# Kernel tuning notes

Hardware: AMD Instinct MI355X
Metric: run time of the kernel (lower is better)

## Reference

```python
import jax, jax.numpy as jnp
import numpy as np

TAU = 0.1

def setup_inputs() -> dict:
    key = jax.random.key(0)
    k1, k2 = jax.random.split(key)
    z_i = jax.random.normal(k1, (4096, 1024), dtype=jnp.float32)
    z_j = jax.random.normal(k2, (4096, 1024), dtype=jnp.float32)
    return {"z_i": z_i, "z_j": z_j}

def reference(z_i, z_j):
    N = z_i.shape[0]
    # L2-normalize each view (world_size=1 so gather is identity)
    k_i = z_i / jnp.linalg.norm(z_i, axis=-1, keepdims=True)
    k_j = z_j / jnp.linalg.norm(z_j, axis=-1, keepdims=True)
    k = jnp.concatenate([k_i, k_j], axis=0)          # [2N, D]
    # cosine similarity of normalized vectors == plain dot products
    sim = k @ k.T                                     # [2N, 2N]
    # positives: (i, i+N) and (i+N, i) pairs
    sim_ij = jnp.diagonal(sim, offset=N)
    sim_ji = jnp.diagonal(sim, offset=-N)
    positives = jnp.concatenate([sim_ij, sim_ji], axis=0)  # [2N]
    # denominator masks out self-similarity on the diagonal
    mask = ~jnp.eye(2 * N, dtype=bool)
    denom = jnp.sum(jnp.where(mask, jnp.exp(sim / TAU), 0.0), axis=1)  # [2N]
    all_losses = -(positives / TAU - jnp.log(denom))
    loss = jnp.sum(all_losses) / (2 * N)
    return loss
```

## Files before the change

### kernel.cpp

```cpp
#include <hip/hip_runtime.h>
#include <hip/hip_bf16.h>
#include <cstdint>
#include <math.h>

#define D_DIM 1024
#define TAU_INV 10.0f
#define EXP_SCALE (TAU_INV / 4096.0f)
#define BK 64
#define NT (D_DIM / BK)
#define BM 256
#define BN 128
#define SLOT 24576

typedef float f32x4 __attribute__((ext_vector_type(4)));
typedef long  l64x2 __attribute__((ext_vector_type(2)));

#define VMCNT(n) asm volatile("s_waitcnt vmcnt(" #n ")" ::: "memory")
#define LGKM0()  asm volatile("s_waitcnt lgkmcnt(0)" ::: "memory")
#define BAR() do { asm volatile("" ::: "memory"); \
                   __builtin_amdgcn_s_barrier();  \
                   asm volatile("" ::: "memory"); } while (0)

__device__ __forceinline__ float wave_reduce_add(float v) {
#pragma unroll
    for (int off = 32; off > 0; off >>= 1) v += __shfl_xor(v, off, 64);
    return v;
}

__global__ __launch_bounds__(256)
void norm_pos_kernel(const float* __restrict__ zi, const float* __restrict__ zj,
                     unsigned int* __restrict__ Kf, float* __restrict__ rowsum,
                     float* __restrict__ pos, int n_half) {
    const int i = blockIdx.x;
    const int t = threadIdx.x;
    float4 a = reinterpret_cast<const float4*>(zi + (size_t)i * D_DIM)[t];
    float4 b = reinterpret_cast<const float4*>(zj + (size_t)i * D_DIM)[t];
    float ssa = a.x*a.x + a.y*a.y + a.z*a.z + a.w*a.w;
    float ssb = b.x*b.x + b.y*b.y + b.z*b.z + b.w*b.w;
    float dab = a.x*b.x + a.y*b.y + a.z*b.z + a.w*b.w;
    ssa = wave_reduce_add(ssa);
    ssb = wave_reduce_add(ssb);
    dab = wave_reduce_add(dab);
    __shared__ float wsa[4], wsb[4], wsd[4];
    if ((t & 63) == 0) { wsa[t>>6] = ssa; wsb[t>>6] = ssb; wsd[t>>6] = dab; }
    __syncthreads();
    const float inva = 1.0f / sqrtf(wsa[0] + wsa[1] + wsa[2] + wsa[3]);
    const float invb = 1.0f / sqrtf(wsb[0] + wsb[1] + wsb[2] + wsb[3]);
    const float sa = inva * 64.0f;
    const float sb = invb * 64.0f;
    unsigned int ua = 0, ub = 0;
    ua = __builtin_amdgcn_cvt_pk_fp8_f32(a.x * sa, a.y * sa, ua, false);
    ua = __builtin_amdgcn_cvt_pk_fp8_f32(a.z * sa, a.w * sa, ua, true);
    ub = __builtin_amdgcn_cvt_pk_fp8_f32(b.x * sb, b.y * sb, ub, false);
    ub = __builtin_amdgcn_cvt_pk_fp8_f32(b.z * sb, b.w * sb, ub, true);
    const int w = (t >> 4) * 16 + ((t >> 1) & 3) * 4 + ((t >> 3) & 1) * 2 + (t & 1);
    Kf[(size_t)i * 256 + w] = ua;
    Kf[(size_t)(i + n_half) * 256 + w] = ub;
    if (t == 0) {
        pos[i] = (wsd[0] + wsd[1] + wsd[2] + wsd[3]) * inva * invb;
        rowsum[i] = 0.0f;
        rowsum[i + n_half] = 0.0f;
    }
}

__global__ __launch_bounds__(512, 4)
void simclr_gemm_kernel(const unsigned char* __restrict__ Kmat,
                        float* __restrict__ rowsum, int n_total) {
    __shared__ char lds[73728];

    const int tid  = threadIdx.x;
    const int lane = tid & 63;
    const int wave = tid >> 6;
    const int wr = wave >> 1;
    const int wc = wave & 1;
    const int kgrp = lane >> 4;

    const int wg = (blockIdx.x & 7) * 132 + (blockIdx.x >> 3);

    int by = 0, start = 0;
    while (wg >= start + (64 - 2 * by)) { start += 64 - 2 * by; ++by; }
    const int bx = 2 * by + (wg - start);
    const bool diag = ((bx >> 1) == by);
    const int rowbase = by * BM;
    const int colbase = bx * BN;

    const char* gK = reinterpret_cast<const char*>(Kmat);
    const int srow = tid >> 2;
    const int sswz = (tid & 3) ^ ((srow >> 1) & 3);

    auto stage_all = [&](int tt) {
        const int s = tt % 3;
        const size_t kbyte = (size_t)tt * BK;
        char* dstA = lds + s * SLOT + tid * 16;
        char* dstB = lds + s * SLOT + 16384 + tid * 16;
#pragma unroll
        for (int i = 0; i < 2; ++i) {
            const int row = i * 128 + srow;
            const char* src = gK + (size_t)(rowbase + row) * D_DIM + kbyte + sswz * 16;
            __builtin_amdgcn_global_load_lds(
                (const __attribute__((address_space(1))) void*)src,
                (__attribute__((address_space(3))) void*)(dstA + i * 8192),
                16, 0, 0);
        }
        {
            const char* src = gK + (size_t)(colbase + srow) * D_DIM + kbyte + sswz * 16;
            __builtin_amdgcn_global_load_lds(
                (const __attribute__((address_space(1))) void*)src,
                (__attribute__((address_space(3))) void*)dstB,
                16, 0, 0);
        }
    };

    f32x4 acc[4][4] = {};
    l64x2 af[4], bf[4];

    auto read_frag = [&](const char* base, int row) -> l64x2 {
        return *reinterpret_cast<const l64x2*>(
            base + row * 64 + ((kgrp ^ ((row >> 1) & 3)) << 4));
    };

    stage_all(0); stage_all(1);
    VMCNT(3); BAR();

    for (int t = 0; t < NT; ++t) {
        const int s = t % 3;
        const char* Ab = lds + s * SLOT;
        const char* Bb = Ab + 16384;
#pragma unroll
        for (int mi = 0; mi < 4; ++mi)
            af[mi] = read_frag(Ab, wr * 64 + mi * 16 + (lane & 15));
#pragma unroll
        for (int ni = 0; ni < 4; ++ni)
            bf[ni] = read_frag(Bb, wc * 64 + ni * 16 + (lane & 15));
        if (t + 2 < NT) stage_all(t + 2);
        __builtin_amdgcn_s_setprio(1);
#pragma unroll
        for (int mi = 0; mi < 4; ++mi)
#pragma unroll
            for (int ni = 0; ni < 4; ++ni)
                acc[mi][ni] = __builtin_amdgcn_mfma_f32_16x16x32_fp8_fp8(
                    af[mi].x, bf[ni].x, acc[mi][ni], 0, 0, 0);
        __builtin_amdgcn_s_setprio(0);
        if (t < NT - 1) {
            LGKM0();
            if (t < NT - 2) { VMCNT(3); } else { VMCNT(0); }
            BAR();
        }
        __builtin_amdgcn_s_setprio(1);
#pragma unroll
        for (int mi = 0; mi < 4; ++mi)
#pragma unroll
            for (int ni = 0; ni < 4; ++ni)
                acc[mi][ni] = __builtin_amdgcn_mfma_f32_16x16x32_fp8_fp8(
                    af[mi].y, bf[ni].y, acc[mi][ni], 0, 0, 0);
        __builtin_amdgcn_s_setprio(0);
    }

    float colpart[4] = {0.0f, 0.0f, 0.0f, 0.0f};
#pragma unroll
    for (int mi = 0; mi < 4; ++mi) {
#pragma unroll
        for (int reg = 0; reg < 4; ++reg) {
            const int grow = rowbase + wr * 64 + mi * 16 + ((lane >> 4) << 2) + reg;
            float rowpart = 0.0f;
#pragma unroll
            for (int ni = 0; ni < 4; ++ni) {
                const int gcol = colbase + wc * 64 + ni * 16 + (lane & 15);
                float e = __expf(acc[mi][ni][reg] * EXP_SCALE);
                if (diag && grow == gcol) e = 0.0f;
                rowpart += e;
                colpart[ni] += e;
            }
#pragma unroll
            for (int off = 1; off < 16; off <<= 1)
                rowpart += __shfl_xor(rowpart, off, 64);
            if ((lane & 15) == 0) atomicAdd(&rowsum[grow], rowpart);
        }
    }
    if (!diag) {
#pragma unroll
        for (int ni = 0; ni < 4; ++ni) {
            float cp = colpart[ni];
            cp += __shfl_xor(cp, 16, 64);
            cp += __shfl_xor(cp, 32, 64);
            if (lane < 16)
                atomicAdd(&rowsum[colbase + wc * 64 + ni * 16 + lane], cp);
        }
    }
}

__global__ __launch_bounds__(256)
void loss_kernel(const float* __restrict__ rowsum, const float* __restrict__ pos,
                 float* __restrict__ out, int n_total, int n_half) {
    const int t = threadIdx.x;
    float acc = 0.0f;
    for (int r = t; r < n_total; r += 256) {
        const int pi = (r < n_half) ? r : (r - n_half);
        acc += logf(rowsum[r]) - TAU_INV * pos[pi];
    }
    acc = wave_reduce_add(acc);
    __shared__ float ws4[4];
    if ((t & 63) == 0) ws4[t >> 6] = acc;
    __syncthreads();
    if (t == 0) out[0] = (ws4[0] + ws4[1] + ws4[2] + ws4[3]) / (float)n_total;
}

extern "C" void kernel_launch(void* const* d_in, const int* in_sizes, int n_in,
                              void* d_out, int out_size, void* d_ws, size_t ws_size,
                              hipStream_t stream) {
    const float* zi = (const float*)d_in[0];
    const float* zj = (const float*)d_in[1];
    float* out = (float*)d_out;

    const int n_half  = in_sizes[0] / D_DIM;
    const int n_total = 2 * n_half;

    char* ws = (char*)d_ws;
    unsigned int* Kf = (unsigned int*)ws;
    size_t off = (size_t)n_total * D_DIM;
    float* rowsum = (float*)(ws + off); off += (size_t)n_total * 4;
    float* pos    = (float*)(ws + off); off += (size_t)n_half * 4;

    norm_pos_kernel<<<n_half, 256, 0, stream>>>(zi, zj, Kf, rowsum, pos, n_half);

    simclr_gemm_kernel<<<1056, 512, 0, stream>>>((const unsigned char*)Kf,
                                                 rowsum, n_total);

    loss_kernel<<<1, 256, 0, stream>>>(rowsum, pos, out, n_total, n_half);
}
```

Baseline: 82.07 us.

## Double-buffer LDS fragment registers in GEMM and parallelize final loss reduction

```diff
diff --git a/kernel.cpp b/kernel.cpp
--- a/kernel.cpp
+++ b/kernel.cpp
@@ -30,7 +30,7 @@
 __global__ __launch_bounds__(256)
 void norm_pos_kernel(const float* __restrict__ zi, const float* __restrict__ zj,
                      unsigned int* __restrict__ Kf, float* __restrict__ rowsum,
-                     float* __restrict__ pos, int n_half) {
+                     float* __restrict__ pos, float* __restrict__ out, int n_half) {
     const int i = blockIdx.x;
     const int t = threadIdx.x;
     float4 a = reinterpret_cast<const float4*>(zi + (size_t)i * D_DIM)[t];
@@ -60,6 +60,7 @@
         pos[i] = (wsd[0] + wsd[1] + wsd[2] + wsd[3]) * inva * invb;
         rowsum[i] = 0.0f;
         rowsum[i + n_half] = 0.0f;
+        if (i == 0) out[0] = 0.0f;
     }
 }
 
@@ -112,18 +113,13 @@
     };
 
     f32x4 acc[4][4] = {};
-    l64x2 af[4], bf[4];
+    l64x2 afA[4], bfA[4], afB[4], bfB[4];
 
     auto read_frag = [&](const char* base, int row) -> l64x2 {
         return *reinterpret_cast<const l64x2*>(
             base + row * 64 + ((kgrp ^ ((row >> 1) & 3)) << 4));
     };
-
-    stage_all(0); stage_all(1);
-    VMCNT(3); BAR();
-
-    for (int t = 0; t < NT; ++t) {
-        const int s = t % 3;
+    auto readAB = [&](int s, l64x2* af, l64x2* bf) {
         const char* Ab = lds + s * SLOT;
         const char* Bb = Ab + 16384;
 #pragma unroll
@@ -132,7 +128,8 @@
 #pragma unroll
         for (int ni = 0; ni < 4; ++ni)
             bf[ni] = read_frag(Bb, wc * 64 + ni * 16 + (lane & 15));
-        if (t + 2 < NT) stage_all(t + 2);
+    };
+    auto mma_lo = [&](const l64x2* af, const l64x2* bf) {
         __builtin_amdgcn_s_setprio(1);
 #pragma unroll
         for (int mi = 0; mi < 4; ++mi)
@@ -141,11 +138,8 @@
                 acc[mi][ni] = __builtin_amdgcn_mfma_f32_16x16x32_fp8_fp8(
                     af[mi].x, bf[ni].x, acc[mi][ni], 0, 0, 0);
         __builtin_amdgcn_s_setprio(0);
-        if (t < NT - 1) {
-            LGKM0();
-            if (t < NT - 2) { VMCNT(3); } else { VMCNT(0); }
-            BAR();
-        }
+    };
+    auto mma_hi = [&](const l64x2* af, const l64x2* bf) {
         __builtin_amdgcn_s_setprio(1);
 #pragma unroll
         for (int mi = 0; mi < 4; ++mi)
@@ -154,6 +148,31 @@
                 acc[mi][ni] = __builtin_amdgcn_mfma_f32_16x16x32_fp8_fp8(
                     af[mi].y, bf[ni].y, acc[mi][ni], 0, 0, 0);
         __builtin_amdgcn_s_setprio(0);
+    };
+
+    stage_all(0); stage_all(1);
+    VMCNT(3); BAR();
+    readAB(0, afA, bfA);
+
+#pragma unroll
+    for (int tt = 0; tt < NT / 2; ++tt) {
+        const int t = 2 * tt;
+        if (t + 2 < NT) stage_all(t + 2);
+        mma_lo(afA, bfA);
+        LGKM0();
+        if (t < NT - 2) { VMCNT(3); } else { VMCNT(0); }
+        BAR();
+        readAB((t + 1) % 3, afB, bfB);
+        mma_hi(afA, bfA);
+        if (t + 3 < NT) stage_all(t + 3);
+        mma_lo(afB, bfB);
+        if (t + 1 < NT - 1) {
+            LGKM0();
+            if (t + 1 < NT - 2) { VMCNT(3); } else { VMCNT(0); }
+            BAR();
+            readAB((t + 2) % 3, afA, bfA);
+        }
+        mma_hi(afB, bfB);
     }
 
     float colpart[4] = {0.0f, 0.0f, 0.0f, 0.0f};
@@ -193,16 +212,15 @@
 void loss_kernel(const float* __restrict__ rowsum, const float* __restrict__ pos,
                  float* __restrict__ out, int n_total, int n_half) {
     const int t = threadIdx.x;
-    float acc = 0.0f;
-    for (int r = t; r < n_total; r += 256) {
-        const int pi = (r < n_half) ? r : (r - n_half);
-        acc += logf(rowsum[r]) - TAU_INV * pos[pi];
-    }
-    acc = wave_reduce_add(acc);
+    const int r = blockIdx.x * 256 + t;
+    const int pi = (r < n_half) ? r : (r - n_half);
+    float v = logf(rowsum[r]) - TAU_INV * pos[pi];
+    v = wave_reduce_add(v);
     __shared__ float ws4[4];
-    if ((t & 63) == 0) ws4[t >> 6] = acc;
+    if ((t & 63) == 0) ws4[t >> 6] = v;
     __syncthreads();
-    if (t == 0) out[0] = (ws4[0] + ws4[1] + ws4[2] + ws4[3]) / (float)n_total;
+    if (t == 0)
+        atomicAdd(out, (ws4[0] + ws4[1] + ws4[2] + ws4[3]) / (float)n_total);
 }
 
 extern "C" void kernel_launch(void* const* d_in, const int* in_sizes, int n_in,
@@ -221,10 +239,10 @@
     float* rowsum = (float*)(ws + off); off += (size_t)n_total * 4;
     float* pos    = (float*)(ws + off); off += (size_t)n_half * 4;
 
-    norm_pos_kernel<<<n_half, 256, 0, stream>>>(zi, zj, Kf, rowsum, pos, n_half);
+    norm_pos_kernel<<<n_half, 256, 0, stream>>>(zi, zj, Kf, rowsum, pos, out, n_half);
 
     simclr_gemm_kernel<<<1056, 512, 0, stream>>>((const unsigned char*)Kf,
                                                  rowsum, n_total);
 
-    loss_kernel<<<1, 256, 0, stream>>>(rowsum, pos, out, n_total, n_half);
-}
+    loss_kernel<<<n_total / 256, 256, 0, stream>>>(rowsum, pos, out, n_total, n_half);
+}
```

Measured after the change: 196.3 us. 139% more time.

## Split-K the first tile row across extra blocks and parallelize loss reduction

Applied to the files above, without the earlier changes.

```diff
diff --git a/kernel.cpp b/kernel.cpp
--- a/kernel.cpp
+++ b/kernel.cpp
@@ -11,6 +11,7 @@
 #define BM 256
 #define BN 128
 #define SLOT 24576
+#define NSPLIT 32
 
 typedef float f32x4 __attribute__((ext_vector_type(4)));
 typedef long  l64x2 __attribute__((ext_vector_type(2)));
@@ -30,7 +31,8 @@
 __global__ __launch_bounds__(256)
 void norm_pos_kernel(const float* __restrict__ zi, const float* __restrict__ zj,
                      unsigned int* __restrict__ Kf, float* __restrict__ rowsum,
-                     float* __restrict__ pos, int n_half) {
+                     float* __restrict__ pos, float* __restrict__ Sq,
+                     float* __restrict__ out, int n_half) {
     const int i = blockIdx.x;
     const int t = threadIdx.x;
     float4 a = reinterpret_cast<const float4*>(zi + (size_t)i * D_DIM)[t];
@@ -56,16 +58,19 @@
     const int w = (t >> 4) * 16 + ((t >> 1) & 3) * 4 + ((t >> 3) & 1) * 2 + (t & 1);
     Kf[(size_t)i * 256 + w] = ua;
     Kf[(size_t)(i + n_half) * 256 + w] = ub;
+    Sq[(size_t)i * 256 + t] = 0.0f;
     if (t == 0) {
         pos[i] = (wsd[0] + wsd[1] + wsd[2] + wsd[3]) * inva * invb;
         rowsum[i] = 0.0f;
         rowsum[i + n_half] = 0.0f;
+        if (i == 0) out[0] = 0.0f;
     }
 }
 
 __global__ __launch_bounds__(512, 4)
 void simclr_gemm_kernel(const unsigned char* __restrict__ Kmat,
-                        float* __restrict__ rowsum, int n_total) {
+                        float* __restrict__ rowsum, float* __restrict__ Sq,
+                        int n_total) {
     __shared__ char lds[73728];
 
     const int tid  = threadIdx.x;
@@ -75,22 +80,35 @@
     const int wc = wave & 1;
     const int kgrp = lane >> 4;
 
-    const int wg = (blockIdx.x & 7) * 132 + (blockIdx.x >> 3);
-
-    int by = 0, start = 0;
-    while (wg >= start + (64 - 2 * by)) { start += 64 - 2 * by; ++by; }
-    const int bx = 2 * by + (wg - start);
-    const bool diag = ((bx >> 1) == by);
-    const int rowbase = by * BM;
-    const int colbase = bx * BN;
+    int rowbase, colbase, k0, stile = 0;
+    bool diag = false, quarter;
+    if (blockIdx.x < 1024) {
+        const int wg = 32 + ((blockIdx.x & 7) * 128 + (blockIdx.x >> 3));
+        int by = 0, start = 0;
+        while (wg >= start + (64 - 2 * by)) { start += 64 - 2 * by; ++by; }
+        const int bx = 2 * by + (wg - start);
+        diag = ((bx >> 1) == by);
+        rowbase = by * BM;
+        colbase = bx * BN;
+        k0 = 0;
+        quarter = false;
+    } else {
+        const int r = blockIdx.x - 1024;
+        stile = r >> 2;
+        const int q = r & 3;
+        rowbase = 0;
+        colbase = stile * BN;
+        k0 = q * 4;
+        quarter = true;
+    }
 
     const char* gK = reinterpret_cast<const char*>(Kmat);
     const int srow = tid >> 2;
     const int sswz = (tid & 3) ^ ((srow >> 1) & 3);
 
-    auto stage_all = [&](int tt) {
-        const int s = tt % 3;
-        const size_t kbyte = (size_t)tt * BK;
+    auto stage_all = [&](int a) {
+        const int s = a % 3;
+        const size_t kbyte = (size_t)a * BK;
         char* dstA = lds + s * SLOT + tid * 16;
         char* dstB = lds + s * SLOT + 16384 + tid * 16;
 #pragma unroll
@@ -119,73 +137,121 @@
             base + row * 64 + ((kgrp ^ ((row >> 1) & 3)) << 4));
     };
 
-    stage_all(0); stage_all(1);
-    VMCNT(3); BAR();
-
-    for (int t = 0; t < NT; ++t) {
-        const int s = t % 3;
-        const char* Ab = lds + s * SLOT;
-        const char* Bb = Ab + 16384;
-#pragma unroll
-        for (int mi = 0; mi < 4; ++mi)
-            af[mi] = read_frag(Ab, wr * 64 + mi * 16 + (lane & 15));
-#pragma unroll
-        for (int ni = 0; ni < 4; ++ni)
-            bf[ni] = read_frag(Bb, wc * 64 + ni * 16 + (lane & 15));
-        if (t + 2 < NT) stage_all(t + 2);
-        __builtin_amdgcn_s_setprio(1);
-#pragma unroll
-        for (int mi = 0; mi < 4; ++mi)
+    auto run = [&](int kk0, int knt) {
+        stage_all(kk0); stage_all(kk0 + 1);
+        VMCNT(3); BAR();
+        for (int t = 0; t < knt; ++t) {
+            const int a = kk0 + t;
+            const int s = a % 3;
+            const char* Ab = lds + s * SLOT;
+            const char* Bb = Ab + 16384;
+#pragma unroll
+            for (int mi = 0; mi < 4; ++mi)
+                af[mi] = read_frag(Ab, wr * 64 + mi * 16 + (lane & 15));
 #pragma unroll
             for (int ni = 0; ni < 4; ++ni)
-                acc[mi][ni] = __builtin_amdgcn_mfma_f32_16x16x32_fp8_fp8(
-                    af[mi].x, bf[ni].x, acc[mi][ni], 0, 0, 0);
-        __builtin_amdgcn_s_setprio(0);
-        if (t < NT - 1) {
-            LGKM0();
-            if (t < NT - 2) { VMCNT(3); } else { VMCNT(0); }
-            BAR();
-        }
-        __builtin_amdgcn_s_setprio(1);
-#pragma unroll
-        for (int mi = 0; mi < 4; ++mi)
-#pragma unroll
-            for (int ni = 0; ni < 4; ++ni)
-                acc[mi][ni] = __builtin_amdgcn_mfma_f32_16x16x32_fp8_fp8(
-                    af[mi].y, bf[ni].y, acc[mi][ni], 0, 0, 0);
-        __builtin_amdgcn_s_setprio(0);
-    }
-
-    float colpart[4] = {0.0f, 0.0f, 0.0f, 0.0f};
-#pragma unroll
-    for (int mi = 0; mi < 4; ++mi) {
-#pragma unroll
-        for (int reg = 0; reg < 4; ++reg) {
-            const int grow = rowbase + wr * 64 + mi * 16 + ((lane >> 4) << 2) + reg;
-            float rowpart = 0.0f;
+                bf[ni] = read_frag(Bb, wc * 64 + ni * 16 + (lane & 15));
+            if (t + 2 < knt) stage_all(a + 2);
+            __builtin_amdgcn_s_setprio(1);
+#pragma unroll
+            for (int mi = 0; mi < 4; ++mi)
+#pragma unroll
+                for (int ni = 0; ni < 4; ++ni)
+                    acc[mi][ni] = __builtin_amdgcn_mfma_f32_16x16x32_fp8_fp8(
+                        af[mi].x, bf[ni].x, acc[mi][ni], 0, 0, 0);
+            __builtin_amdgcn_s_setprio(0);
+            if (t < knt - 1) {
+                LGKM0();
+                if (t < knt - 2) { VMCNT(3); } else { VMCNT(0); }
+                BAR();
+            }
+            __builtin_amdgcn_s_setprio(1);
+#pragma unroll
+            for (int mi = 0; mi < 4; ++mi)
+#pragma unroll
+                for (int ni = 0; ni < 4; ++ni)
+                    acc[mi][ni] = __builtin_amdgcn_mfma_f32_16x16x32_fp8_fp8(
+                        af[mi].y, bf[ni].y, acc[mi][ni], 0, 0, 0);
+            __builtin_amdgcn_s_setprio(0);
+        }
+    };
+
+    if (!quarter) {
+        run(0, NT);
+        float colpart[4] = {0.0f, 0.0f, 0.0f, 0.0f};
+#pragma unroll
+        for (int mi = 0; mi < 4; ++mi) {
+#pragma unroll
+            for (int reg = 0; reg < 4; ++reg) {
+                const int grow = rowbase + wr * 64 + mi * 16 + ((lane >> 4) << 2) + reg;
+                float rowpart = 0.0f;
+#pragma unroll
+                for (int ni = 0; ni < 4; ++ni) {
+                    const int gcol = colbase + wc * 64 + ni * 16 + (lane & 15);
+                    float e = __expf(acc[mi][ni][reg] * EXP_SCALE);
+                    if (diag && grow == gcol) e = 0.0f;
+                    rowpart += e;
+                    colpart[ni] += e;
+                }
+#pragma unroll
+                for (int off = 1; off < 16; off <<= 1)
+                    rowpart += __shfl_xor(rowpart, off, 64);
+                if ((lane & 15) == 0) atomicAdd(&rowsum[grow], rowpart);
+            }
+        }
+        if (!diag) {
 #pragma unroll
             for (int ni = 0; ni < 4; ++ni) {
-                const int gcol = colbase + wc * 64 + ni * 16 + (lane & 15);
-                float e = __expf(acc[mi][ni][reg] * EXP_SCALE);
-                if (diag && grow == gcol) e = 0.0f;
-                rowpart += e;
-                colpart[ni] += e;
-            }
-#pragma unroll
-            for (int off = 1; off < 16; off <<= 1)
-                rowpart += __shfl_xor(rowpart, off, 64);
-            if ((lane & 15) == 0) atomicAdd(&rowsum[grow], rowpart);
-        }
-    }
-    if (!diag) {
-#pragma unroll
-        for (int ni = 0; ni < 4; ++ni) {
-            float cp = colpart[ni];
-            cp += __shfl_xor(cp, 16, 64);
-            cp += __shfl_xor(cp, 32, 64);
-            if (lane < 16)
-                atomicAdd(&rowsum[colbase + wc * 64 + ni * 16 + lane], cp);
-        }
+                float cp = colpart[ni];
+                cp += __shfl_xor(cp, 16, 64);
+                cp += __shfl_xor(cp, 32, 64);
+                if (lane < 16)
+                    atomicAdd(&rowsum[colbase + wc * 64 + ni * 16 + lane], cp);
+            }
+        }
+    } else {
+        run(k0, 4);
+        float* St = Sq + (size_t)stile * (BM * BN);
+#pragma unroll
+        for (int mi = 0; mi < 4; ++mi) {
+#pragma unroll
+            for (int reg = 0; reg < 4; ++reg) {
+                const int row = wr * 64 + mi * 16 + ((lane >> 4) << 2) + reg;
+#pragma unroll
+                for (int ni = 0; ni < 4; ++ni) {
+                    const int col = wc * 64 + ni * 16 + (lane & 15);
+                    atomicAdd(&St[row * BN + col], acc[mi][ni][reg]);
+                }
+            }
+        }
+    }
+}
+
+__global__ __launch_bounds__(512)
+void fixup_kernel(const float* __restrict__ Sq, float* __restrict__ rowsum) {
+    const int s = blockIdx.x;
+    const int lane = threadIdx.x & 63;
+    const int wave = threadIdx.x >> 6;
+    const float* St = Sq + (size_t)s * (BM * BN);
+    const bool dtile = (s < 2);
+    float cp0 = 0.0f, cp1 = 0.0f;
+    for (int i = 0; i < 32; ++i) {
+        const int r = wave * 32 + i;
+        float e0 = __expf(St[r * BN + lane] * EXP_SCALE);
+        float e1 = __expf(St[r * BN + 64 + lane] * EXP_SCALE);
+        if (dtile) {
+            if (r == s * BN + lane) e0 = 0.0f;
+            if (r == s * BN + 64 + lane) e1 = 0.0f;
+        }
+        float rp = e0 + e1;
+#pragma unroll
+        for (int off = 1; off < 64; off <<= 1) rp += __shfl_xor(rp, off, 64);
+        if (lane == 0) atomicAdd(&rowsum[r], rp);
+        cp0 += e0; cp1 += e1;
+    }
+    if (!dtile) {
+        atomicAdd(&rowsum[s * BN + lane], cp0);
+        atomicAdd(&rowsum[s * BN + 64 + lane], cp1);
     }
 }
 
@@ -193,16 +259,15 @@
 void loss_kernel(const float* __restrict__ rowsum, const float* __restrict__ pos,
                  float* __restrict__ out, int n_total, int n_half) {
     const int t = threadIdx.x;
-    float acc = 0.0f;
-    for (int r = t; r < n_total; r += 256) {
-        const int pi = (r < n_half) ? r : (r - n_half);
-        acc += logf(rowsum[r]) - TAU_INV * pos[pi];
-    }
-    acc = wave_reduce_add(acc);
+    const int r = blockIdx.x * 256 + t;
+    const int pi = (r < n_half) ? r : (r - n_half);
+    float v = logf(rowsum[r]) - TAU_INV * pos[pi];
+    v = wave_reduce_add(v);
     __shared__ float ws4[4];
-    if ((t & 63) == 0) ws4[t >> 6] = acc;
+    if ((t & 63) == 0) ws4[t >> 6] = v;
     __syncthreads();
-    if (t == 0) out[0] = (ws4[0] + ws4[1] + ws4[2] + ws4[3]) / (float)n_total;
+    if (t == 0)
+        atomicAdd(out, (ws4[0] + ws4[1] + ws4[2] + ws4[3]) / (float)n_total);
 }
 
 extern "C" void kernel_launch(void* const* d_in, const int* in_sizes, int n_in,
@@ -218,13 +283,16 @@
     char* ws = (char*)d_ws;
     unsigned int* Kf = (unsigned int*)ws;
     size_t off = (size_t)n_total * D_DIM;
+    float* Sq     = (float*)(ws + off); off += (size_t)NSPLIT * BM * BN * 4;
     float* rowsum = (float*)(ws + off); off += (size_t)n_total * 4;
     float* pos    = (float*)(ws + off); off += (size_t)n_half * 4;
 
-    norm_pos_kernel<<<n_half, 256, 0, stream>>>(zi, zj, Kf, rowsum, pos, n_half);
-
-    simclr_gemm_kernel<<<1056, 512, 0, stream>>>((const unsigned char*)Kf,
-                                                 rowsum, n_total);
-
-    loss_kernel<<<1, 256, 0, stream>>>(rowsum, pos, out, n_total, n_half);
-}
+    norm_pos_kernel<<<n_half, 256, 0, stream>>>(zi, zj, Kf, rowsum, pos, Sq, out, n_half);
+
+    simclr_gemm_kernel<<<1024 + 4 * NSPLIT, 512, 0, stream>>>(
+        (const unsigned char*)Kf, rowsum, Sq, n_total);
+
+    fixup_kernel<<<NSPLIT, 512, 0, stream>>>(Sq, rowsum);
+
+    loss_kernel<<<n_total / 256, 256, 0, stream>>>(rowsum, pos, out, n_total, n_half);
+}
```

New measurement: 99.49 us. 21.2% more time.
